# Optimization experiments

Hardware: AMD Instinct MI355X
Metric: run time of the kernel (lower is better)

The kernel has to match this reference:

```python
import jax, jax.numpy as jnp
import numpy as np
from jax import lax

B, DIM, H, DM, NH = 32, 16, 128, 256, 8  # batch, in-channels, seq, d_model, n_head


def setup_inputs() -> dict:
    key = jax.random.key(0)
    k1, k2, k3, k4, k5 = jax.random.split(key, 5)
    x = jax.random.normal(k1, (B, DIM, H, DM), jnp.float32)
    conv1_w = jax.random.normal(k2, (3 * NH * DIM, 1, 5, 1), jnp.float32) * 0.1
    conv2_w = jax.random.normal(k3, (3 * NH * DIM, 1, 1, NH), jnp.float32) * 0.1
    w_out_w = jax.random.normal(k4, (DM, DM), jnp.float32) * (1.0 / np.sqrt(DM))
    w_out_b = jax.random.normal(k5, (DM,), jnp.float32) * 0.01
    return dict(x=x, conv1_w=conv1_w, conv2_w=conv2_w, w_out_w=w_out_w, w_out_b=w_out_b)


def reference(x, conv1_w, conv2_w, w_out_w, w_out_b):
    b, dim, h, w = x.shape
    nh = conv2_w.shape[-1]
    dn = ('NCHW', 'OIHW', 'NCHW')
    # grouped conv (5,1), padding 'same' on height, groups=dim
    y = lax.conv_general_dilated(x, conv1_w, (1, 1), [(2, 2), (0, 0)],
                                 dimension_numbers=dn, feature_group_count=dim)
    # depthwise conv (1, nh) stride (1, nh): width w -> w/nh
    y = lax.conv_general_dilated(y, conv2_w, (1, nh), [(0, 0), (0, 0)],
                                 dimension_numbers=dn, feature_group_count=y.shape[1])
    # dropout layers are identity in eval mode
    C = nh * dim
    wp = w // nh
    y = y.reshape(b, 3, C, h, wp)  # 'b (n c) h w -> n b c h w' split, n=3 outer
    q, k, v = y[:, 0], y[:, 1], y[:, 2]  # each [b, C, h, wp]
    scores = jnp.einsum('bcqd,bckd->bcqk', q, k) / jnp.sqrt(jnp.float32(wp))
    attn = jax.nn.softmax(scores, axis=-1)
    o = jnp.einsum('bcqk,bckd->bcqd', attn, v)  # [b, C, h, wp]
    # 'b (c n) h w -> b c h (n w)' with c=dim, n=nh
    o = o.reshape(b, dim, nh, h, wp).transpose(0, 1, 3, 2, 4).reshape(b, dim, h, nh * wp)
    return o @ w_out_w.T + w_out_b
```

## Files before the change

### kernel.cpp

```cpp
#include <hip/hip_runtime.h>
#include <stdint.h>

#define B_   32
#define DIM_ 16
#define H_   128
#define DM_  256
#define NH_  8
#define WP_  32
#define C3_  384

typedef short bf16x8 __attribute__((ext_vector_type(8)));
typedef float f32x4  __attribute__((ext_vector_type(4)));

__device__ __forceinline__ unsigned short f2bfu(float v) {
    unsigned int x = __float_as_uint(v);
    x += 0x7fffu + ((x >> 16) & 1u);
    return (unsigned short)(x >> 16);
}
__device__ __forceinline__ unsigned cvtpk(float lo, float hi) {
    unsigned r;
    asm("v_cvt_pk_bf16_f32 %0, %1, %2" : "=v"(r) : "v"(lo), "v"(hi));
    return r;
}
__device__ __forceinline__ void gl_lds16(const void* g, void* l) {
    __builtin_amdgcn_global_load_lds(
        (const __attribute__((address_space(1))) unsigned int*)g,
        (__attribute__((address_space(3))) unsigned int*)l, 16, 0, 0);
}
__device__ __forceinline__ void tr2(const void* p, uint2& r0, uint2& r1) {
    const __attribute__((address_space(3))) unsigned char* lp =
        (const __attribute__((address_space(3))) unsigned char*)p;
    asm volatile("s_waitcnt lgkmcnt(0)\n\t"
                 "ds_read_b64_tr_b16 %0, %2\n\t"
                 "ds_read_b64_tr_b16 %1, %2 offset:512\n\t"
                 "s_waitcnt lgkmcnt(0)"
                 : "=v"(r0), "=v"(r1) : "v"(lp) : "memory");
}

__global__ __launch_bounds__(256) void conv_kernel(
    const float* __restrict__ x, const float* __restrict__ w1,
    const float* __restrict__ w2, unsigned short* __restrict__ y2)
{
    __shared__ float wlds[24 * 16];
    __shared__ __align__(16) unsigned char tbuf[4][1024];

    const int bid = blockIdx.x;
    const int ht = bid & 1;
    const int g  = (bid >> 1) & 15;
    const int b  = bid >> 5;
    const int tid = threadIdx.x;
    const int wp = tid & 31;
    const int hl = tid >> 5;
    const int h0 = ht * 64 + hl * 8;
    const int lane = tid & 63, wv = tid >> 6;

    for (int i = tid; i < 384; i += 256) {
        const int oc = i >> 4, ix = i & 15;
        const int o = g * 24 + oc;
        float v = 0.f;
        if (ix < 5)       v = w1[o * 5 + ix];
        else if (ix < 13) v = w2[o * 8 + (ix - 5)];
        wlds[i] = v;
    }

    const float* xbase = x + ((size_t)(b * DIM_ + g) * H_) * DM_ + wp * 8;

    float xr[12][8];
    #pragma unroll
    for (int r = 0; r < 12; ++r) {
        const int hr = h0 - 2 + r;
        if (hr >= 0 && hr < H_) {
            const float4* p = (const float4*)(xbase + (size_t)hr * DM_);
            float4 a = p[0], c = p[1];
            xr[r][0] = a.x; xr[r][1] = a.y; xr[r][2] = a.z; xr[r][3] = a.w;
            xr[r][4] = c.x; xr[r][5] = c.y; xr[r][6] = c.z; xr[r][7] = c.w;
        } else {
            #pragma unroll
            for (int j = 0; j < 8; ++j) xr[r][j] = 0.f;
        }
    }
    __syncthreads();

    unsigned char* tw = &tbuf[wv][0];
    const unsigned wbo = (((lane >> 5) * 8) + 16 * (wp & 3)
                        + 256 * ((wp >> 2) & 1) + 64 * (wp >> 3)) * 2;
    const unsigned rdo = ((lane & 15) + 64 * (lane >> 4)) * 2;
    const int h_s  = ht * 64 + wv * 16 + (lane & 15);
    const int wp_s = (lane >> 4) * 8;

    for (int oc = 0; oc < 24; ++oc) {
        const int o = g * 24 + oc;
        const float* wo_ = &wlds[oc * 16];
        float w1r[5], w2r[8];
        {
            float4 a = *(const float4*)(wo_);
            float4 c = *(const float4*)(wo_ + 4);
            float4 d = *(const float4*)(wo_ + 8);
            w1r[0] = a.x; w1r[1] = a.y; w1r[2] = a.z; w1r[3] = a.w;
            w1r[4] = c.x;
            w2r[0] = c.y; w2r[1] = c.z; w2r[2] = c.w;
            w2r[3] = d.x; w2r[4] = d.y; w2r[5] = d.z; w2r[6] = d.w;
            w2r[7] = wo_[12];
        }

        float u[12];
        #pragma unroll
        for (int r = 0; r < 12; ++r) {
            float s = w2r[0] * xr[r][0];
            #pragma unroll
            for (int j = 1; j < 8; ++j) s = fmaf(w2r[j], xr[r][j], s);
            u[r] = s;
        }

        float ys[8];
        #pragma unroll
        for (int hh = 0; hh < 8; ++hh) {
            float y = w1r[0] * u[hh];
            #pragma unroll
            for (int t = 1; t < 5; ++t) y = fmaf(w1r[t], u[hh + t], y);
            ys[hh] = y;
        }
        uint4 pk;
        pk.x = cvtpk(ys[0], ys[1]); pk.y = cvtpk(ys[2], ys[3]);
        pk.z = cvtpk(ys[4], ys[5]); pk.w = cvtpk(ys[6], ys[7]);

        if (o >= 256) {
            *(uint4*)(y2 + ((size_t)(b * C3_ + o) * 32 + wp) * 128 + h0) = pk;
        } else {
            *(uint4*)(tw + wbo) = pk;
            uint2 r0, r1;
            tr2(tw + rdo, r0, r1);
            *(uint4*)(y2 + ((size_t)(b * C3_ + o) * 128 + h_s) * 32 + wp_s) =
                make_uint4(r0.x, r0.y, r1.x, r1.y);
        }
    }
}

__global__ __launch_bounds__(256) void attn_kernel(
    const unsigned short* __restrict__ y2, unsigned short* __restrict__ z)
{
    __shared__ __align__(16) unsigned char sm[40960];

    const int tid = threadIdx.x;
    const int ch = blockIdx.x & 127, b = blockIdx.x >> 7;
    const size_t base = ((size_t)(b * C3_ + ch)) * 4096;
    const uint4* qg = (const uint4*)(y2 + base);
    const uint4* kg = (const uint4*)(y2 + base + 128 * 4096);
    const uint4* vg = (const uint4*)(y2 + base + 256 * 4096);

    #pragma unroll
    for (int r = 0; r < 2; ++r) {
        const int ci  = tid + r * 256;
        const int row = ci >> 2;
        const int c   = ci & 3;
        const int cx  = c ^ ((row >> 1) & 3);
        *(uint4*)(sm + row * 64 + cx * 16)        = qg[ci];
        *(uint4*)(sm + 8192 + row * 64 + cx * 16) = kg[ci];
        const int vd = ci >> 4;
        const int vhc = ci & 15;
        *(uint4*)(sm + 32768 + vd * 256 + ((vhc * 16) ^ ((vd & 7) << 4))) = vg[ci];
    }
    __syncthreads();

    const int l  = tid & 63, wv = tid >> 6;
    const int lm = l & 15,  lk = l >> 4;

    bf16x8 qf[2];
    #pragma unroll
    for (int t = 0; t < 2; ++t) {
        const int q = (wv * 2 + t) * 16 + lm;
        qf[t] = *(const bf16x8*)(sm + q * 64 + ((lk ^ ((q >> 1) & 3)) << 4));
    }
    f32x4 acc[8][2];
    #pragma unroll
    for (int rt = 0; rt < 8; ++rt) {
        acc[rt][0] = 0; acc[rt][1] = 0;
    }
    #pragma unroll
    for (int rt = 0; rt < 8; ++rt) {
        const int kr = rt * 16 + lm;
        bf16x8 kf = *(const bf16x8*)(sm + 8192 + kr * 64 + ((lk ^ ((kr >> 1) & 3)) << 4));
        acc[rt][0] = __builtin_amdgcn_mfma_f32_16x16x32_bf16(kf, qf[0], acc[rt][0], 0, 0, 0);
        acc[rt][1] = __builtin_amdgcn_mfma_f32_16x16x32_bf16(kf, qf[1], acc[rt][1], 0, 0, 0);
    }

    const float Cc = 0.17677669529663687f * 1.4426950408889634f;
    float inv[2];
    #pragma unroll
    for (int t = 0; t < 2; ++t) {
        float m = acc[0][t][0];
        #pragma unroll
        for (int rt = 0; rt < 8; ++rt)
            #pragma unroll
            for (int rg = 0; rg < 4; ++rg) m = fmaxf(m, acc[rt][t][rg]);
        m = fmaxf(m, __shfl_xor(m, 16));
        m = fmaxf(m, __shfl_xor(m, 32));
        float s = 0.f;
        #pragma unroll
        for (int rt = 0; rt < 8; ++rt)
            #pragma unroll
            for (int rg = 0; rg < 4; ++rg) {
                float p = exp2f((acc[rt][t][rg] - m) * Cc);
                acc[rt][t][rg] = p; s += p;
            }
        s += __shfl_xor(s, 16);
        s += __shfl_xor(s, 32);
        inv[t] = 1.0f / s;
    }

    __syncthreads();

    #pragma unroll
    for (int t = 0; t < 2; ++t) {
        const int q = (wv * 2 + t) * 16 + lm;
        #pragma unroll
        for (int rt = 0; rt < 8; ++rt) {
            unsigned u0 = cvtpk(acc[rt][t][0] * inv[t], acc[rt][t][1] * inv[t]);
            unsigned u1 = cvtpk(acc[rt][t][2] * inv[t], acc[rt][t][3] * inv[t]);
            const int kb = rt * 32 + lk * 8;
            *(uint2*)(sm + q * 256 + (kb ^ ((q & 7) << 4))) = make_uint2(u0, u1);
        }
    }
    __syncthreads();

    f32x4 o[2][2];
    o[0][0] = 0; o[0][1] = 0; o[1][0] = 0; o[1][1] = 0;
    #pragma unroll
    for (int kc = 0; kc < 4; ++kc) {
        const int cb = kc * 64 + lk * 16;
        bf16x8 av[2], bp[2];
        #pragma unroll
        for (int dt = 0; dt < 2; ++dt) {
            const int d = dt * 16 + lm;
            av[dt] = *(const bf16x8*)(sm + 32768 + d * 256 + (cb ^ ((d & 7) << 4)));
        }
        #pragma unroll
        for (int t = 0; t < 2; ++t) {
            const int q = (wv * 2 + t) * 16 + lm;
            bp[t] = *(const bf16x8*)(sm + q * 256 + (cb ^ ((q & 7) << 4)));
        }
        #pragma unroll
        for (int dt = 0; dt < 2; ++dt)
            #pragma unroll
            for (int t = 0; t < 2; ++t)
                o[dt][t] = __builtin_amdgcn_mfma_f32_16x16x32_bf16(av[dt], bp[t], o[dt][t], 0, 0, 0);
    }

    const int dd = ch >> 3, nn = ch & 7;
    unsigned short* zb = z + ((size_t)(b * DIM_ + dd)) * (H_ * DM_);
    #pragma unroll
    for (int dt = 0; dt < 2; ++dt)
        #pragma unroll
        for (int t = 0; t < 2; ++t) {
            const int q  = (wv * 2 + t) * 16 + lm;
            const int d0 = dt * 16 + lk * 4;
            unsigned u0 = cvtpk(o[dt][t][0], o[dt][t][1]);
            unsigned u1 = cvtpk(o[dt][t][2], o[dt][t][3]);
            *(uint2*)(zb + (size_t)q * DM_ + nn * 32 + d0) = make_uint2(u0, u1);
        }
}

__global__ __launch_bounds__(256) void prep_w(
    const float* __restrict__ w, unsigned short* __restrict__ wh,
    unsigned short* __restrict__ wl)
{
    const int i = blockIdx.x * 1024 + threadIdx.x * 4;
    float4 v = *(const float4*)(w + i);
    float vv[4] = { v.x, v.y, v.z, v.w };
    unsigned short h[4], lo[4];
    #pragma unroll
    for (int j = 0; j < 4; ++j) {
        h[j] = f2bfu(vv[j]);
        float hf = __uint_as_float(((unsigned)h[j]) << 16);
        lo[j] = f2bfu(vv[j] - hf);
    }
    *(uint2*)(wh + i) = make_uint2((unsigned)h[0] | ((unsigned)h[1] << 16),
                                   (unsigned)h[2] | ((unsigned)h[3] << 16));
    *(uint2*)(wl + i) = make_uint2((unsigned)lo[0] | ((unsigned)lo[1] << 16),
                                   (unsigned)lo[2] | ((unsigned)lo[3] << 16));
}

__global__ __launch_bounds__(256) void proj_kernel(
    const unsigned short* __restrict__ zz, const unsigned short* __restrict__ wh,
    const unsigned short* __restrict__ wl, const float* __restrict__ bias,
    float* __restrict__ out)
{
    __shared__ __align__(16) unsigned char sm[65536];
    const int tid = threadIdx.x;
    const int l = tid & 63, wv = tid >> 6, lm = l & 15, lk = l >> 4;
    const unsigned short* zs = zz + (size_t)blockIdx.x * 32768;

    const int g_off = (tid >> 2) * 256 + (tid & 3) * 8;
    const int lds_wv = wv * 1024;

    const int arow0 = wv * 32 + lm;

    f32x4 acc[2][16];
    #pragma unroll
    for (int t = 0; t < 2; ++t)
        #pragma unroll
        for (int nt = 0; nt < 16; ++nt) acc[t][nt] = 0;

    bf16x8 areg[2][2];

    #pragma unroll
    for (int i = 0; i < 8; ++i) {
        const unsigned short* g = (i < 4 ? wh : wl) + g_off + (i & 3) * 16384;
        gl_lds16(g, sm + i * 4096 + lds_wv);
    }
    #pragma unroll
    for (int t = 0; t < 2; ++t)
        areg[0][t] = *(const bf16x8*)(zs + (size_t)(arow0 + t * 16) * 256 + lk * 8);

    __syncthreads();

    #pragma unroll
    for (int kc = 0; kc < 8; ++kc) {
        const int buf = kc & 1;
        if (kc < 7) {
            #pragma unroll
            for (int i = 0; i < 8; ++i) {
                const unsigned short* g = (i < 4 ? wh : wl) + g_off + (i & 3) * 16384 + (kc + 1) * 32;
                gl_lds16(g, sm + (buf ^ 1) * 32768 + i * 4096 + lds_wv);
            }
            #pragma unroll
            for (int t = 0; t < 2; ++t)
                areg[buf ^ 1][t] = *(const bf16x8*)(zs + (size_t)(arow0 + t * 16) * 256 + (kc + 1) * 32 + lk * 8);
        }
        #pragma unroll
        for (int ph = 0; ph < 2; ++ph)
            #pragma unroll
            for (int nt = 0; nt < 16; ++nt) {
                bf16x8 bf = *(const bf16x8*)(sm + buf * 32768 + ph * 16384 + nt * 1024 + lm * 64 + lk * 16);
                acc[0][nt] = __builtin_amdgcn_mfma_f32_16x16x32_bf16(areg[buf][0], bf, acc[0][nt], 0, 0, 0);
                acc[1][nt] = __builtin_amdgcn_mfma_f32_16x16x32_bf16(areg[buf][1], bf, acc[1][nt], 0, 0, 0);
            }
        __syncthreads();
    }

    float* ob = out + (size_t)blockIdx.x * 32768;
    #pragma unroll
    for (int t = 0; t < 2; ++t)
        #pragma unroll
        for (int nt = 0; nt < 16; ++nt) {
            const float bv = bias[nt * 16 + lm];
            #pragma unroll
            for (int rg = 0; rg < 4; ++rg)
                ob[(size_t)(wv * 32 + t * 16 + lk * 4 + rg) * 256 + nt * 16 + lm] = acc[t][nt][rg] + bv;
        }
}

extern "C" void kernel_launch(void* const* d_in, const int* in_sizes, int n_in,
                              void* d_out, int out_size, void* d_ws, size_t ws_size,
                              hipStream_t stream)
{
    const float* x  = (const float*)d_in[0];
    const float* w1 = (const float*)d_in[1];
    const float* w2 = (const float*)d_in[2];
    const float* wo = (const float*)d_in[3];
    const float* wb = (const float*)d_in[4];
    float* out = (float*)d_out;

    unsigned short* y2 = (unsigned short*)d_ws;
    unsigned short* zz = y2 + (size_t)B_ * C3_ * H_ * WP_;
    unsigned short* wh = y2;
    unsigned short* wl = y2 + 65536;

    conv_kernel<<<dim3(1024), dim3(256), 0, stream>>>(x, w1, w2, y2);
    attn_kernel<<<dim3(4096), dim3(256), 0, stream>>>(y2, zz);
    prep_w<<<dim3(64), dim3(256), 0, stream>>>(wo, wh, wl);
    proj_kernel<<<dim3(512), dim3(256), 0, stream>>>(zz, wh, wl, wb, out);
}
```

Baseline: 114.2 us.

## Split conv output channels across two thread halves; vectorize projection epilogue stores

The conv kernel now runs 512 threads per block, with each half computing 12 of the 24 output channels. This doubles parallelism per block and halves the serial channel loop, at the cost of each half loading the same input rows redundantly. Separately, the projection MFMA operands are swapped so each lane holds 4 consecutive output columns, which lets the epilogue use float4 bias loads and float4 stores instead of scalar strided stores.

```diff
diff --git a/kernel.cpp b/kernel.cpp
--- a/kernel.cpp
+++ b/kernel.cpp
@@ -37,30 +37,33 @@
                  : "=v"(r0), "=v"(r1) : "v"(lp) : "memory");
 }
 
-__global__ __launch_bounds__(256) void conv_kernel(
+__global__ __launch_bounds__(512) void conv_kernel(
     const float* __restrict__ x, const float* __restrict__ w1,
     const float* __restrict__ w2, unsigned short* __restrict__ y2)
 {
     __shared__ float wlds[24 * 16];
-    __shared__ __align__(16) unsigned char tbuf[4][1024];
+    __shared__ __align__(16) unsigned char tbuf[8][1024];
 
     const int bid = blockIdx.x;
     const int ht = bid & 1;
     const int g  = (bid >> 1) & 15;
     const int b  = bid >> 5;
     const int tid = threadIdx.x;
-    const int wp = tid & 31;
-    const int hl = tid >> 5;
+    const int ocs = tid >> 8;
+    const int tl  = tid & 255;
+    const int wp = tl & 31;
+    const int hl = tl >> 5;
     const int h0 = ht * 64 + hl * 8;
+    const int oc0 = ocs * 12;
     const int lane = tid & 63, wv = tid >> 6;
 
-    for (int i = tid; i < 384; i += 256) {
-        const int oc = i >> 4, ix = i & 15;
+    if (tid < 384) {
+        const int oc = tid >> 4, ix = tid & 15;
         const int o = g * 24 + oc;
         float v = 0.f;
         if (ix < 5)       v = w1[o * 5 + ix];
         else if (ix < 13) v = w2[o * 8 + (ix - 5)];
-        wlds[i] = v;
+        wlds[tid] = v;
     }
 
     const float* xbase = x + ((size_t)(b * DIM_ + g) * H_) * DM_ + wp * 8;
@@ -85,12 +88,12 @@
     const unsigned wbo = (((lane >> 5) * 8) + 16 * (wp & 3)
                         + 256 * ((wp >> 2) & 1) + 64 * (wp >> 3)) * 2;
     const unsigned rdo = ((lane & 15) + 64 * (lane >> 4)) * 2;
-    const int h_s  = ht * 64 + wv * 16 + (lane & 15);
+    const int h_s  = ht * 64 + (wv & 3) * 16 + (lane & 15);
     const int wp_s = (lane >> 4) * 8;
 
-    for (int oc = 0; oc < 24; ++oc) {
-        const int o = g * 24 + oc;
-        const float* wo_ = &wlds[oc * 16];
+    for (int ocl = 0; ocl < 12; ++ocl) {
+        const int o = g * 24 + oc0 + ocl;
+        const float* wo_ = &wlds[(oc0 + ocl) * 16];
         float w1r[5], w2r[8];
         {
             float4 a = *(const float4*)(wo_);
@@ -332,22 +335,25 @@
             #pragma unroll
             for (int nt = 0; nt < 16; ++nt) {
                 bf16x8 bf = *(const bf16x8*)(sm + buf * 32768 + ph * 16384 + nt * 1024 + lm * 64 + lk * 16);
-                acc[0][nt] = __builtin_amdgcn_mfma_f32_16x16x32_bf16(areg[buf][0], bf, acc[0][nt], 0, 0, 0);
-                acc[1][nt] = __builtin_amdgcn_mfma_f32_16x16x32_bf16(areg[buf][1], bf, acc[1][nt], 0, 0, 0);
+                acc[0][nt] = __builtin_amdgcn_mfma_f32_16x16x32_bf16(bf, areg[buf][0], acc[0][nt], 0, 0, 0);
+                acc[1][nt] = __builtin_amdgcn_mfma_f32_16x16x32_bf16(bf, areg[buf][1], acc[1][nt], 0, 0, 0);
             }
         __syncthreads();
     }
 
     float* ob = out + (size_t)blockIdx.x * 32768;
     #pragma unroll
-    for (int t = 0; t < 2; ++t)
+    for (int t = 0; t < 2; ++t) {
+        const int row = wv * 32 + t * 16 + lm;
         #pragma unroll
         for (int nt = 0; nt < 16; ++nt) {
-            const float bv = bias[nt * 16 + lm];
-            #pragma unroll
-            for (int rg = 0; rg < 4; ++rg)
-                ob[(size_t)(wv * 32 + t * 16 + lk * 4 + rg) * 256 + nt * 16 + lm] = acc[t][nt][rg] + bv;
-        }
+            const int col = nt * 16 + lk * 4;
+            const float4 bv = *(const float4*)(bias + col);
+            float4 vv = make_float4(acc[t][nt][0] + bv.x, acc[t][nt][1] + bv.y,
+                                    acc[t][nt][2] + bv.z, acc[t][nt][3] + bv.w);
+            *(float4*)&ob[(size_t)row * 256 + col] = vv;
+        }
+    }
 }
 
 extern "C" void kernel_launch(void* const* d_in, const int* in_sizes, int n_in,
@@ -366,7 +372,7 @@
     unsigned short* wh = y2;
     unsigned short* wl = y2 + 65536;
 
-    conv_kernel<<<dim3(1024), dim3(256), 0, stream>>>(x, w1, w2, y2);
+    conv_kernel<<<dim3(1024), dim3(512), 0, stream>>>(x, w1, w2, y2);
     attn_kernel<<<dim3(4096), dim3(256), 0, stream>>>(y2, zz);
     prep_w<<<dim3(64), dim3(256), 0, stream>>>(wo, wh, wl);
     proj_kernel<<<dim3(512), dim3(256), 0, stream>>>(zz, wh, wl, wb, out);
```

Result: faster. 111.1 us (-2.8%).

## Store Q/K in conv-native layout, transpose in attention LDS, vectorize output stores

Applied to the files above, without the earlier changes.

The conv kernel now writes all Q/K/V channels in the same h-contiguous layout, removing the per-channel LDS transpose and its wait barriers from the conv loop. The attention kernel instead scatters Q and K into LDS in a transpose-friendly order and reads MFMA fragments with ds_read_b64_tr_b16. The final projection swaps the MFMA operand order so each lane holds four consecutive output columns, allowing float4 bias loads and float4 stores. The transpose cost moves into attention, and its helper's waitcnt(0) calls may serialize the LDS reads there.

```diff
diff --git a/kernel.cpp b/kernel.cpp
--- a/kernel.cpp
+++ b/kernel.cpp
@@ -36,13 +36,17 @@
                  "s_waitcnt lgkmcnt(0)"
                  : "=v"(r0), "=v"(r1) : "v"(lp) : "memory");
 }
+__device__ __forceinline__ bf16x8 mk8(uint2 r0, uint2 r1) {
+    union { uint4 u; bf16x8 v; } c;
+    c.u = make_uint4(r0.x, r0.y, r1.x, r1.y);
+    return c.v;
+}
 
 __global__ __launch_bounds__(256) void conv_kernel(
     const float* __restrict__ x, const float* __restrict__ w1,
     const float* __restrict__ w2, unsigned short* __restrict__ y2)
 {
     __shared__ float wlds[24 * 16];
-    __shared__ __align__(16) unsigned char tbuf[4][1024];
 
     const int bid = blockIdx.x;
     const int ht = bid & 1;
@@ -52,7 +56,6 @@
     const int wp = tid & 31;
     const int hl = tid >> 5;
     const int h0 = ht * 64 + hl * 8;
-    const int lane = tid & 63, wv = tid >> 6;
 
     for (int i = tid; i < 384; i += 256) {
         const int oc = i >> 4, ix = i & 15;
@@ -81,15 +84,9 @@
     }
     __syncthreads();
 
-    unsigned char* tw = &tbuf[wv][0];
-    const unsigned wbo = (((lane >> 5) * 8) + 16 * (wp & 3)
-                        + 256 * ((wp >> 2) & 1) + 64 * (wp >> 3)) * 2;
-    const unsigned rdo = ((lane & 15) + 64 * (lane >> 4)) * 2;
-    const int h_s  = ht * 64 + wv * 16 + (lane & 15);
-    const int wp_s = (lane >> 4) * 8;
+    unsigned short* yb = y2 + ((size_t)(b * C3_ + g * 24) * 32 + wp) * 128 + h0;
 
     for (int oc = 0; oc < 24; ++oc) {
-        const int o = g * 24 + oc;
         const float* wo_ = &wlds[oc * 16];
         float w1r[5], w2r[8];
         {
@@ -123,16 +120,7 @@
         uint4 pk;
         pk.x = cvtpk(ys[0], ys[1]); pk.y = cvtpk(ys[2], ys[3]);
         pk.z = cvtpk(ys[4], ys[5]); pk.w = cvtpk(ys[6], ys[7]);
-
-        if (o >= 256) {
-            *(uint4*)(y2 + ((size_t)(b * C3_ + o) * 32 + wp) * 128 + h0) = pk;
-        } else {
-            *(uint4*)(tw + wbo) = pk;
-            uint2 r0, r1;
-            tr2(tw + rdo, r0, r1);
-            *(uint4*)(y2 + ((size_t)(b * C3_ + o) * 128 + h_s) * 32 + wp_s) =
-                make_uint4(r0.x, r0.y, r1.x, r1.y);
-        }
+        *(uint4*)(yb + (size_t)oc * 4096) = pk;
     }
 }
 
@@ -151,25 +139,26 @@
     #pragma unroll
     for (int r = 0; r < 2; ++r) {
         const int ci  = tid + r * 256;
-        const int row = ci >> 2;
-        const int c   = ci & 3;
-        const int cx  = c ^ ((row >> 1) & 3);
-        *(uint4*)(sm + row * 64 + cx * 16)        = qg[ci];
-        *(uint4*)(sm + 8192 + row * 64 + cx * 16) = kg[ci];
-        const int vd = ci >> 4;
+        const int vd  = ci >> 4;
         const int vhc = ci & 15;
+        const int toff = (vhc >> 1) * 1024 +
+            ((((vhc & 1) * 8) + 16 * (vd & 3) + 256 * ((vd >> 2) & 1) + 64 * (vd >> 3)) << 1);
+        *(uint4*)(sm + toff)        = qg[ci];
+        *(uint4*)(sm + 8192 + toff) = kg[ci];
         *(uint4*)(sm + 32768 + vd * 256 + ((vhc * 16) ^ ((vd & 7) << 4))) = vg[ci];
     }
     __syncthreads();
 
     const int l  = tid & 63, wv = tid >> 6;
     const int lm = l & 15,  lk = l >> 4;
+    const unsigned rdo = ((l & 15) + 64 * (l >> 4)) * 2;
 
     bf16x8 qf[2];
     #pragma unroll
     for (int t = 0; t < 2; ++t) {
-        const int q = (wv * 2 + t) * 16 + lm;
-        qf[t] = *(const bf16x8*)(sm + q * 64 + ((lk ^ ((q >> 1) & 3)) << 4));
+        uint2 r0, r1;
+        tr2(sm + (wv * 2 + t) * 1024 + rdo, r0, r1);
+        qf[t] = mk8(r0, r1);
     }
     f32x4 acc[8][2];
     #pragma unroll
@@ -178,8 +167,9 @@
     }
     #pragma unroll
     for (int rt = 0; rt < 8; ++rt) {
-        const int kr = rt * 16 + lm;
-        bf16x8 kf = *(const bf16x8*)(sm + 8192 + kr * 64 + ((lk ^ ((kr >> 1) & 3)) << 4));
+        uint2 r0, r1;
+        tr2(sm + 8192 + rt * 1024 + rdo, r0, r1);
+        bf16x8 kf = mk8(r0, r1);
         acc[rt][0] = __builtin_amdgcn_mfma_f32_16x16x32_bf16(kf, qf[0], acc[rt][0], 0, 0, 0);
         acc[rt][1] = __builtin_amdgcn_mfma_f32_16x16x32_bf16(kf, qf[1], acc[rt][1], 0, 0, 0);
     }
@@ -332,22 +322,25 @@
             #pragma unroll
             for (int nt = 0; nt < 16; ++nt) {
                 bf16x8 bf = *(const bf16x8*)(sm + buf * 32768 + ph * 16384 + nt * 1024 + lm * 64 + lk * 16);
-                acc[0][nt] = __builtin_amdgcn_mfma_f32_16x16x32_bf16(areg[buf][0], bf, acc[0][nt], 0, 0, 0);
-                acc[1][nt] = __builtin_amdgcn_mfma_f32_16x16x32_bf16(areg[buf][1], bf, acc[1][nt], 0, 0, 0);
+                acc[0][nt] = __builtin_amdgcn_mfma_f32_16x16x32_bf16(bf, areg[buf][0], acc[0][nt], 0, 0, 0);
+                acc[1][nt] = __builtin_amdgcn_mfma_f32_16x16x32_bf16(bf, areg[buf][1], acc[1][nt], 0, 0, 0);
             }
         __syncthreads();
     }
 
     float* ob = out + (size_t)blockIdx.x * 32768;
     #pragma unroll
-    for (int t = 0; t < 2; ++t)
+    for (int t = 0; t < 2; ++t) {
+        const int row = wv * 32 + t * 16 + lm;
         #pragma unroll
         for (int nt = 0; nt < 16; ++nt) {
-            const float bv = bias[nt * 16 + lm];
-            #pragma unroll
-            for (int rg = 0; rg < 4; ++rg)
-                ob[(size_t)(wv * 32 + t * 16 + lk * 4 + rg) * 256 + nt * 16 + lm] = acc[t][nt][rg] + bv;
-        }
+            const int col = nt * 16 + lk * 4;
+            const float4 bv = *(const float4*)(bias + col);
+            float4 vv = make_float4(acc[t][nt][0] + bv.x, acc[t][nt][1] + bv.y,
+                                    acc[t][nt][2] + bv.z, acc[t][nt][3] + bv.w);
+            *(float4*)&ob[(size_t)row * 256 + col] = vv;
+        }
+    }
 }
 
 extern "C" void kernel_launch(void* const* d_in, const int* in_sizes, int n_in,
```

Result: slower. 122.2 us (+7.0%).
